# Performance work log

Measured on AMD Instinct MI355X. Metric: run time of the kernel, lower is better.

## Reference

```python
import jax, jax.numpy as jnp
import numpy as np

N, K, D = 131072, 1024, 128


def setup_inputs() -> dict:
    key = jax.random.key(0)
    k1, k2 = jax.random.split(key)
    latent = jax.random.normal(k1, (N, D), dtype=jnp.float32)
    coords = jax.random.uniform(k2, (K, D), dtype=jnp.float32)  # torch.rand init
    return {"latent": latent, "coords": coords}


def reference(latent, coords):
    # Euclidean cdist argmin: sqrt is monotone, so argmin of squared distances
    # matches torch.cdist(...).min(1)[1].
    x2 = jnp.sum(latent * latent, axis=1, keepdims=True)          # [N, 1]
    c2 = jnp.sum(coords * coords, axis=1)[None, :]                # [1, K]
    d2 = x2 + c2 - 2.0 * (latent @ coords.T)                      # [N, K]
    closest_centroid = jnp.argmin(d2, axis=1)                     # [N] int
    # original also computes cluster_distances but discards it; output is indices
    return closest_centroid
```

## Files before the change

### kernel.cpp

```cpp
#include <hip/hip_runtime.h>


constexpr int N = 131072;
constexpr int K = 1024;
constexpr int D = 128;
constexpr float EPS2 = 0.06f;

typedef __attribute__((ext_vector_type(8))) short short8;
typedef __attribute__((ext_vector_type(4))) float f32x4;

typedef const __attribute__((address_space(1))) uint* gas_uint;
typedef __attribute__((address_space(3))) uint* las_uint;

union U8 { uint4 u; short8 s; };
__device__ inline short8 as_s8(uint4 v) { U8 x; x.u = v; return x.s; }

__device__ inline uint bf16rne(float f) {
    uint u = __float_as_uint(f);
    return (u + 0x7fffu + ((u >> 16) & 1u)) >> 16;
}
__device__ inline void split2(float a, float b, uint& hi, uint& lo) {
    uint ha = bf16rne(a), hb = bf16rne(b);
    float la = a - __uint_as_float(ha << 16);
    float lb = b - __uint_as_float(hb << 16);
    hi = ha | (hb << 16);
    lo = bf16rne(la) | (bf16rne(lb) << 16);
}

__global__ __launch_bounds__(256) void prep_kernel(
    const float* __restrict__ coords, float* __restrict__ c2half,
    uint* __restrict__ chilo, int* __restrict__ counter) {
    if (blockIdx.x == 0 && threadIdx.x == 0) counter[0] = 0;
    const int k = blockIdx.x * 4 + (threadIdx.x >> 6);
    const int dw = threadIdx.x & 63;
    float a = coords[k * D + 2 * dw], b = coords[k * D + 2 * dw + 1];
    uint hi, lo;
    split2(a, b, hi, lo);
    const int g = dw >> 2, sub = dw & 3, kt = k >> 5, m = k & 31;
    char* base = (char*)chilo + (size_t)kt * 16384 + m * 256 +
                 ((g ^ (m & 15)) << 4) + sub * 4;
    *(uint*)base = hi;
    *(uint*)(base + 8192) = lo;
    float s = fmaf(a, a, b * b);
#pragma unroll
    for (int off = 1; off < 64; off <<= 1) s += __shfl_xor(s, off);
    if (dw == 0) c2half[k] = 0.5f * s;
}

__global__ __launch_bounds__(256) void transpose_kernel(
    const float* __restrict__ coords, float* __restrict__ coordsT) {
    __shared__ float tile[64][65];
    const int k0 = blockIdx.x * 64;
    const int d0 = blockIdx.y * 64;
    const int tx = threadIdx.x & 63, ty = threadIdx.x >> 6;
#pragma unroll
    for (int i = 0; i < 64; i += 4)
        tile[ty + i][tx] = coords[(size_t)(k0 + ty + i) * D + d0 + tx];
    __syncthreads();
#pragma unroll
    for (int i = 0; i < 64; i += 4)
        coordsT[(size_t)(d0 + ty + i) * K + k0 + tx] = tile[tx][ty + i];
}

__global__ __launch_bounds__(256, 3) void centroid_mfma_kernel(
    const float* __restrict__ latent, const uint* __restrict__ chilo,
    const float* __restrict__ c2, int* __restrict__ out,
    int* __restrict__ counter, int* __restrict__ list) {
    __shared__ __align__(16) char smem[36864];
    const int tid = threadIdx.x;
    const int l = tid & 63, w = tid >> 6;
    const int l15 = l & 15, l4 = l >> 4;
    const int rowbase = blockIdx.x * 128 + w * 32;

    uint4 bh[2][4], bl[2][4];
#pragma unroll
    for (int grp = 0; grp < 2; ++grp) {
        const float* rp =
            latent + (size_t)(rowbase + grp * 16 + l15) * D + l4 * 8;
#pragma unroll
        for (int s = 0; s < 4; ++s) {
            float4 u = *(const float4*)(rp + 32 * s);
            float4 v = *(const float4*)(rp + 32 * s + 4);
            uint h0, o0, h1, o1, h2, o2, h3, o3;
            split2(-u.x, -u.y, h0, o0);
            split2(-u.z, -u.w, h1, o1);
            split2(-v.x, -v.y, h2, o2);
            split2(-v.z, -v.w, h3, o3);
            bh[grp][s] = make_uint4(h0, h1, h2, h3);
            bl[grp][s] = make_uint4(o0, o1, o2, o3);
        }
    }
    *(float4*)(smem + 32768 + tid * 16) =
        *(const float4*)((const char*)c2 + tid * 16);

    const int w4096 = w << 12;
    const char* gsrc0 = (const char*)chilo + w4096 + ((tid & 63) << 4);
#pragma unroll
    for (int i = 0; i < 4; ++i)
        __builtin_amdgcn_global_load_lds((gas_uint)(gsrc0 + i * 1024),
                                         (las_uint)(smem + w4096 + i * 1024),
                                         16, 0, 0);
#pragma unroll
    for (int i = 0; i < 4; ++i)
        __builtin_amdgcn_global_load_lds((gas_uint)(gsrc0 + 16384 + i * 1024),
                                         (las_uint)(smem + 16384 + w4096 + i * 1024),
                                         16, 0, 0);
    __syncthreads();

    float m1[2] = {3.4e38f, 3.4e38f};
    float m2[2] = {3.4e38f, 3.4e38f};
    uint kpack[8];
#pragma unroll
    for (int ks = 0; ks < 2; ++ks)
#pragma unroll
        for (int r = 0; r < 4; ++r) kpack[ks * 4 + r] = ks * 16 + l4 * 4 + r;
    const float* c2l = (const float*)(smem + 32768);

#pragma unroll 1
    for (int t = 0; t < 32; ++t) {
        const int buf = t & 1;
        if (t < 31)
            asm volatile("s_waitcnt vmcnt(4)" ::: "memory");
        else
            asm volatile("s_waitcnt vmcnt(0)" ::: "memory");
        __builtin_amdgcn_s_barrier();
        __builtin_amdgcn_sched_barrier(0);

        const int k0 = t * 32;
        f32x4 acc[2][2];
#pragma unroll
        for (int ks = 0; ks < 2; ++ks) {
            float4 cq = *(const float4*)(c2l + k0 + ks * 16 + l4 * 4);
#pragma unroll
            for (int grp = 0; grp < 2; ++grp) {
                acc[ks][grp][0] = cq.x;
                acc[ks][grp][1] = cq.y;
                acc[ks][grp][2] = cq.z;
                acc[ks][grp][3] = cq.w;
            }
        }

        const char* lhs = smem + buf * 16384;
        __builtin_amdgcn_s_setprio(1);
#pragma unroll
        for (int s = 0; s < 4; ++s) {
            short8 ahi[2], alo[2];
#pragma unroll
            for (int ks = 0; ks < 2; ++ks) {
                const int m = ks * 16 + l15;
                const int g = l4 + 4 * s;
                const int sw = m * 256 + ((g ^ (m & 15)) << 4);
                ahi[ks] = *(const short8*)(lhs + sw);
                alo[ks] = *(const short8*)(lhs + 8192 + sw);
            }
#pragma unroll
            for (int ks = 0; ks < 2; ++ks) {
#pragma unroll
                for (int grp = 0; grp < 2; ++grp) {
                    acc[ks][grp] = __builtin_amdgcn_mfma_f32_16x16x32_bf16(
                        ahi[ks], as_s8(bh[grp][s]), acc[ks][grp], 0, 0, 0);
                    acc[ks][grp] = __builtin_amdgcn_mfma_f32_16x16x32_bf16(
                        ahi[ks], as_s8(bl[grp][s]), acc[ks][grp], 0, 0, 0);
                    acc[ks][grp] = __builtin_amdgcn_mfma_f32_16x16x32_bf16(
                        alo[ks], as_s8(bh[grp][s]), acc[ks][grp], 0, 0, 0);
                }
            }
        }
        __builtin_amdgcn_s_setprio(0);
        __builtin_amdgcn_sched_barrier(0);

#pragma unroll
        for (int ks = 0; ks < 2; ++ks) {
#pragma unroll
            for (int r = 0; r < 4; ++r) {
                const uint kk = kpack[ks * 4 + r];
#pragma unroll
                for (int grp = 0; grp < 2; ++grp) {
                    uint pb = (__float_as_uint(acc[ks][grp][r]) & 0xFFFFFC00u) | kk;
                    float vp = __uint_as_float(pb);
                    m2[grp] = __builtin_amdgcn_fmed3f(vp, m1[grp], m2[grp]);
                    m1[grp] = fminf(m1[grp], vp);
                }
            }
        }
#pragma unroll
        for (int i = 0; i < 8; ++i) kpack[i] += 32;

        __builtin_amdgcn_s_barrier();
        __builtin_amdgcn_sched_barrier(0);
        if (t < 30) {
            const char* gs = gsrc0 + (size_t)(t + 2) * 16384;
            char* ls = smem + buf * 16384 + w4096;
#pragma unroll
            for (int i = 0; i < 4; ++i)
                __builtin_amdgcn_global_load_lds((gas_uint)(gs + i * 1024),
                                                 (las_uint)(ls + i * 1024),
                                                 16, 0, 0);
        }
    }

#pragma unroll
    for (int off = 16; off <= 32; off <<= 1) {
#pragma unroll
        for (int grp = 0; grp < 2; ++grp) {
            float om = __shfl_xor(m1[grp], off);
            float o2 = __shfl_xor(m2[grp], off);
            m2[grp] = fminf(fminf(m2[grp], o2), fmaxf(m1[grp], om));
            m1[grp] = fminf(m1[grp], om);
        }
    }

    bool flg[2];
    unsigned long long bm[2];
    int total = 0;
#pragma unroll
    for (int grp = 0; grp < 2; ++grp) {
        flg[grp] = (l < 16) && ((m2[grp] - m1[grp]) <= EPS2);
        bm[grp] = __ballot(flg[grp]);
        total += __popcll(bm[grp]);
    }
    int pos = 0;
    if (l == 0 && total) pos = atomicAdd(counter, total);
    pos = __shfl(pos, 0);
    if (l < 16) {
        int run = pos;
#pragma unroll
        for (int grp = 0; grp < 2; ++grp) {
            out[rowbase + grp * 16 + l] = (int)(__float_as_uint(m1[grp]) & 1023u);
            if (flg[grp])
                list[run + __popcll(bm[grp] & ((1ull << l) - 1ull))] =
                    rowbase + grp * 16 + l;
            run += __popcll(bm[grp]);
        }
    }
}

__global__ __launch_bounds__(256) void centroid_exact_kernel(
    const float* __restrict__ latent, const float* __restrict__ coordsT,
    const float* __restrict__ c2, const int* __restrict__ cnt_list,
    int* __restrict__ out) {
    const int count = cnt_list[0];
    const int* list = cnt_list + 16;
    const int lane = threadIdx.x & 63;
    const int gw = (blockIdx.x * 256 + threadIdx.x) >> 6;
    const int nwaves = gridDim.x * 4;

    for (int task = gw; task * 4 < count; task += nwaves) {
        const int base = task * 4;
        const int nr = min(4, count - base);
        const float* xp[4];
        int rows[4];
#pragma unroll
        for (int j = 0; j < 4; ++j) {
            int idx = base + (j < nr ? j : nr - 1);
            rows[j] = __builtin_amdgcn_readfirstlane(list[idx]);
            xp[j] = latent + (size_t)rows[j] * D;
        }

        float acc[16][4];
#pragma unroll
        for (int c = 0; c < 16; ++c) {
            float cc = c2[c * 64 + lane];
#pragma unroll
            for (int j = 0; j < 4; ++j) acc[c][j] = cc;
        }

#pragma unroll 1
        for (int d4 = 0; d4 < D / 4; ++d4) {
            float4 xq[4];
#pragma unroll
            for (int j = 0; j < 4; ++j)
                xq[j] = *(const float4*)(xp[j] + 4 * d4);
            float ct[4][16];
#pragma unroll
            for (int dd = 0; dd < 4; ++dd)
#pragma unroll
                for (int c = 0; c < 16; ++c)
                    ct[dd][c] = coordsT[(size_t)(4 * d4 + dd) * K + c * 64 + lane];
#pragma unroll
            for (int dd = 0; dd < 4; ++dd) {
#pragma unroll
                for (int c = 0; c < 16; ++c) {
#pragma unroll
                    for (int j = 0; j < 4; ++j) {
                        float xv = (dd == 0) ? xq[j].x
                                 : (dd == 1) ? xq[j].y
                                 : (dd == 2) ? xq[j].z : xq[j].w;
                        acc[c][j] = fmaf(-xv, ct[dd][c], acc[c][j]);
                    }
                }
            }
        }

#pragma unroll
        for (int j = 0; j < 4; ++j) {
            float m1 = acc[0][j];
            int i1 = lane;
#pragma unroll
            for (int c = 1; c < 16; ++c) {
                const int kk = c * 64 + lane;
                if (acc[c][j] < m1) { m1 = acc[c][j]; i1 = kk; }
            }
#pragma unroll
            for (int off = 1; off < 64; off <<= 1) {
                float om = __shfl_xor(m1, off);
                int oi = __shfl_xor(i1, off);
                if (om < m1 || (om == m1 && oi < i1)) { m1 = om; i1 = oi; }
            }
            if (lane == 0 && j < nr) out[rows[j]] = i1;
        }
    }
}

extern "C" void kernel_launch(void* const* d_in, const int* in_sizes, int n_in,
                              void* d_out, int out_size, void* d_ws, size_t ws_size,
                              hipStream_t stream) {
    const float* latent = (const float*)d_in[0];
    const float* coords = (const float*)d_in[1];
    int* out = (int*)d_out;

    char* ws = (char*)d_ws;
    size_t off = 0;
    float* c2 = (float*)(ws + off); off += 4096;
    uint* chilo = (uint*)(ws + off); off += 524288;
    float* coordsT = (float*)(ws + off); off += 524288;
    int* cnt_list = (int*)(ws + off); off += 64 + 524288;
    int* counter = cnt_list;
    int* list = cnt_list + 16;

    prep_kernel<<<K / 4, 256, 0, stream>>>(coords, c2, chilo, counter);
    {
        dim3 g(K / 64, D / 64);
        transpose_kernel<<<g, 256, 0, stream>>>(coords, coordsT);
    }
    centroid_mfma_kernel<<<N / 128, 256, 0, stream>>>(latent, chilo, c2, out,
                                                      counter, list);
    centroid_exact_kernel<<<2048, 256, 0, stream>>>(latent, coordsT, c2,
                                                    cnt_list, out);
}
```

Baseline: 151.7 us.

## Switch distance MFMA to single fp16 pass with norm-scaled refine threshold

Replaces the three-pass bf16 hi/lo split GEMM with a single fp16 MFMA pass, which cuts the MFMA work to a third and halves the centroid tile traffic. Blocks become one wave owning 64 rows, so the per-tile workgroup barriers go away and each wave reuses each loaded centroid fragment across four row groups. The near-tie threshold for the exact fallback now scales with each row's norm to cover the larger fp16 error. The risks are more rows sent to the exact kernel and possible fp16 overflow or precision trouble on inputs with a different scale.

```diff
diff --git a/kernel.cpp b/kernel.cpp
--- a/kernel.cpp
+++ b/kernel.cpp
@@ -4,43 +4,35 @@
 constexpr int N = 131072;
 constexpr int K = 1024;
 constexpr int D = 128;
-constexpr float EPS2 = 0.06f;
-
-typedef __attribute__((ext_vector_type(8))) short short8;
+
+typedef __attribute__((ext_vector_type(8))) _Float16 half8;
 typedef __attribute__((ext_vector_type(4))) float f32x4;
 
 typedef const __attribute__((address_space(1))) uint* gas_uint;
 typedef __attribute__((address_space(3))) uint* las_uint;
 
-union U8 { uint4 u; short8 s; };
-__device__ inline short8 as_s8(uint4 v) { U8 x; x.u = v; return x.s; }
-
-__device__ inline uint bf16rne(float f) {
-    uint u = __float_as_uint(f);
-    return (u + 0x7fffu + ((u >> 16) & 1u)) >> 16;
-}
-__device__ inline void split2(float a, float b, uint& hi, uint& lo) {
-    uint ha = bf16rne(a), hb = bf16rne(b);
-    float la = a - __uint_as_float(ha << 16);
-    float lb = b - __uint_as_float(hb << 16);
-    hi = ha | (hb << 16);
-    lo = bf16rne(la) | (bf16rne(lb) << 16);
+union UH { uint4 u; half8 h; };
+__device__ inline half8 as_h8(uint4 v) { UH x; x.u = v; return x.h; }
+
+union H2U { _Float16 h[2]; uint u; };
+__device__ inline uint fp16pk(float a, float b) {
+    H2U x;
+    x.h[0] = (_Float16)a;
+    x.h[1] = (_Float16)b;
+    return x.u;
 }
 
 __global__ __launch_bounds__(256) void prep_kernel(
     const float* __restrict__ coords, float* __restrict__ c2half,
-    uint* __restrict__ chilo, int* __restrict__ counter) {
+    uint* __restrict__ chi, int* __restrict__ counter) {
     if (blockIdx.x == 0 && threadIdx.x == 0) counter[0] = 0;
     const int k = blockIdx.x * 4 + (threadIdx.x >> 6);
     const int dw = threadIdx.x & 63;
     float a = coords[k * D + 2 * dw], b = coords[k * D + 2 * dw + 1];
-    uint hi, lo;
-    split2(a, b, hi, lo);
     const int g = dw >> 2, sub = dw & 3, kt = k >> 5, m = k & 31;
-    char* base = (char*)chilo + (size_t)kt * 16384 + m * 256 +
+    char* base = (char*)chi + (size_t)kt * 8192 + m * 256 +
                  ((g ^ (m & 15)) << 4) + sub * 4;
-    *(uint*)base = hi;
-    *(uint*)(base + 8192) = lo;
+    *(uint*)base = fp16pk(a, b);
     float s = fmaf(a, a, b * b);
 #pragma unroll
     for (int off = 1; off < 64; off <<= 1) s += __shfl_xor(s, off);
@@ -62,77 +54,82 @@
         coordsT[(size_t)(d0 + ty + i) * K + k0 + tx] = tile[tx][ty + i];
 }
 
-__global__ __launch_bounds__(256, 3) void centroid_mfma_kernel(
-    const float* __restrict__ latent, const uint* __restrict__ chilo,
+__global__ __launch_bounds__(64, 2) void centroid_mfma_kernel(
+    const float* __restrict__ latent, const uint* __restrict__ chi,
     const float* __restrict__ c2, int* __restrict__ out,
     int* __restrict__ counter, int* __restrict__ list) {
-    __shared__ __align__(16) char smem[36864];
-    const int tid = threadIdx.x;
-    const int l = tid & 63, w = tid >> 6;
+    __shared__ __align__(16) char smem[20480];
+    const int l = threadIdx.x;
     const int l15 = l & 15, l4 = l >> 4;
-    const int rowbase = blockIdx.x * 128 + w * 32;
-
-    uint4 bh[2][4], bl[2][4];
-#pragma unroll
-    for (int grp = 0; grp < 2; ++grp) {
+    const int rowbase = blockIdx.x * 64;
+
+    uint4 bh[4][4];
+    float n2[4];
+#pragma unroll
+    for (int grp = 0; grp < 4; ++grp) {
         const float* rp =
             latent + (size_t)(rowbase + grp * 16 + l15) * D + l4 * 8;
+        float s2 = 0.f;
 #pragma unroll
         for (int s = 0; s < 4; ++s) {
             float4 u = *(const float4*)(rp + 32 * s);
             float4 v = *(const float4*)(rp + 32 * s + 4);
-            uint h0, o0, h1, o1, h2, o2, h3, o3;
-            split2(-u.x, -u.y, h0, o0);
-            split2(-u.z, -u.w, h1, o1);
-            split2(-v.x, -v.y, h2, o2);
-            split2(-v.z, -v.w, h3, o3);
-            bh[grp][s] = make_uint4(h0, h1, h2, h3);
-            bl[grp][s] = make_uint4(o0, o1, o2, o3);
-        }
-    }
-    *(float4*)(smem + 32768 + tid * 16) =
-        *(const float4*)((const char*)c2 + tid * 16);
-
-    const int w4096 = w << 12;
-    const char* gsrc0 = (const char*)chilo + w4096 + ((tid & 63) << 4);
-#pragma unroll
-    for (int i = 0; i < 4; ++i)
+            s2 += u.x * u.x + u.y * u.y + u.z * u.z + u.w * u.w +
+                  v.x * v.x + v.y * v.y + v.z * v.z + v.w * v.w;
+            bh[grp][s] = make_uint4(fp16pk(-u.x, -u.y), fp16pk(-u.z, -u.w),
+                                    fp16pk(-v.x, -v.y), fp16pk(-v.z, -v.w));
+        }
+        n2[grp] = s2;
+    }
+#pragma unroll
+    for (int grp = 0; grp < 4; ++grp) {
+        n2[grp] += __shfl_xor(n2[grp], 16);
+        n2[grp] += __shfl_xor(n2[grp], 32);
+    }
+
+    {
+        float4* dst = (float4*)(smem + 16384);
+        const float4* src = (const float4*)c2;
+#pragma unroll
+        for (int i = 0; i < 4; ++i) dst[i * 64 + l] = src[i * 64 + l];
+    }
+
+    const char* gsrc0 = (const char*)chi + (l << 4);
+#pragma unroll
+    for (int i = 0; i < 8; ++i)
         __builtin_amdgcn_global_load_lds((gas_uint)(gsrc0 + i * 1024),
-                                         (las_uint)(smem + w4096 + i * 1024),
+                                         (las_uint)(smem + i * 1024), 16, 0, 0);
+#pragma unroll
+    for (int i = 0; i < 8; ++i)
+        __builtin_amdgcn_global_load_lds((gas_uint)(gsrc0 + 8192 + i * 1024),
+                                         (las_uint)(smem + 8192 + i * 1024),
                                          16, 0, 0);
-#pragma unroll
-    for (int i = 0; i < 4; ++i)
-        __builtin_amdgcn_global_load_lds((gas_uint)(gsrc0 + 16384 + i * 1024),
-                                         (las_uint)(smem + 16384 + w4096 + i * 1024),
-                                         16, 0, 0);
-    __syncthreads();
-
-    float m1[2] = {3.4e38f, 3.4e38f};
-    float m2[2] = {3.4e38f, 3.4e38f};
+
+    float m1[4] = {3.4e38f, 3.4e38f, 3.4e38f, 3.4e38f};
+    float m2[4] = {3.4e38f, 3.4e38f, 3.4e38f, 3.4e38f};
     uint kpack[8];
 #pragma unroll
     for (int ks = 0; ks < 2; ++ks)
 #pragma unroll
         for (int r = 0; r < 4; ++r) kpack[ks * 4 + r] = ks * 16 + l4 * 4 + r;
-    const float* c2l = (const float*)(smem + 32768);
+    const float* c2l = (const float*)(smem + 16384);
 
 #pragma unroll 1
     for (int t = 0; t < 32; ++t) {
         const int buf = t & 1;
         if (t < 31)
-            asm volatile("s_waitcnt vmcnt(4)" ::: "memory");
+            asm volatile("s_waitcnt vmcnt(8)" ::: "memory");
         else
             asm volatile("s_waitcnt vmcnt(0)" ::: "memory");
-        __builtin_amdgcn_s_barrier();
         __builtin_amdgcn_sched_barrier(0);
 
         const int k0 = t * 32;
-        f32x4 acc[2][2];
+        f32x4 acc[2][4];
 #pragma unroll
         for (int ks = 0; ks < 2; ++ks) {
             float4 cq = *(const float4*)(c2l + k0 + ks * 16 + l4 * 4);
 #pragma unroll
-            for (int grp = 0; grp < 2; ++grp) {
+            for (int grp = 0; grp < 4; ++grp) {
                 acc[ks][grp][0] = cq.x;
                 acc[ks][grp][1] = cq.y;
                 acc[ks][grp][2] = cq.z;
@@ -140,31 +137,23 @@
             }
         }
 
-        const char* lhs = smem + buf * 16384;
+        const char* lhs = smem + buf * 8192;
         __builtin_amdgcn_s_setprio(1);
 #pragma unroll
         for (int s = 0; s < 4; ++s) {
-            short8 ahi[2], alo[2];
+            half8 a[2];
 #pragma unroll
             for (int ks = 0; ks < 2; ++ks) {
                 const int m = ks * 16 + l15;
                 const int g = l4 + 4 * s;
-                const int sw = m * 256 + ((g ^ (m & 15)) << 4);
-                ahi[ks] = *(const short8*)(lhs + sw);
-                alo[ks] = *(const short8*)(lhs + 8192 + sw);
-            }
-#pragma unroll
-            for (int ks = 0; ks < 2; ++ks) {
-#pragma unroll
-                for (int grp = 0; grp < 2; ++grp) {
-                    acc[ks][grp] = __builtin_amdgcn_mfma_f32_16x16x32_bf16(
-                        ahi[ks], as_s8(bh[grp][s]), acc[ks][grp], 0, 0, 0);
-                    acc[ks][grp] = __builtin_amdgcn_mfma_f32_16x16x32_bf16(
-                        ahi[ks], as_s8(bl[grp][s]), acc[ks][grp], 0, 0, 0);
-                    acc[ks][grp] = __builtin_amdgcn_mfma_f32_16x16x32_bf16(
-                        alo[ks], as_s8(bh[grp][s]), acc[ks][grp], 0, 0, 0);
-                }
-            }
+                a[ks] = *(const half8*)(lhs + m * 256 + ((g ^ (m & 15)) << 4));
+            }
+#pragma unroll
+            for (int ks = 0; ks < 2; ++ks)
+#pragma unroll
+                for (int grp = 0; grp < 4; ++grp)
+                    acc[ks][grp] = __builtin_amdgcn_mfma_f32_16x16x32_f16(
+                        a[ks], as_h8(bh[grp][s]), acc[ks][grp], 0, 0, 0);
         }
         __builtin_amdgcn_s_setprio(0);
         __builtin_amdgcn_sched_barrier(0);
@@ -175,7 +164,7 @@
             for (int r = 0; r < 4; ++r) {
                 const uint kk = kpack[ks * 4 + r];
 #pragma unroll
-                for (int grp = 0; grp < 2; ++grp) {
+                for (int grp = 0; grp < 4; ++grp) {
                     uint pb = (__float_as_uint(acc[ks][grp][r]) & 0xFFFFFC00u) | kk;
                     float vp = __uint_as_float(pb);
                     m2[grp] = __builtin_amdgcn_fmed3f(vp, m1[grp], m2[grp]);
@@ -186,13 +175,13 @@
 #pragma unroll
         for (int i = 0; i < 8; ++i) kpack[i] += 32;
 
-        __builtin_amdgcn_s_barrier();
+        asm volatile("s_waitcnt lgkmcnt(0)" ::: "memory");
         __builtin_amdgcn_sched_barrier(0);
         if (t < 30) {
-            const char* gs = gsrc0 + (size_t)(t + 2) * 16384;
-            char* ls = smem + buf * 16384 + w4096;
-#pragma unroll
-            for (int i = 0; i < 4; ++i)
+            const char* gs = gsrc0 + (size_t)(t + 2) * 8192;
+            char* ls = smem + buf * 8192;
+#pragma unroll
+            for (int i = 0; i < 8; ++i)
                 __builtin_amdgcn_global_load_lds((gas_uint)(gs + i * 1024),
                                                  (las_uint)(ls + i * 1024),
                                                  16, 0, 0);
@@ -202,7 +191,7 @@
 #pragma unroll
     for (int off = 16; off <= 32; off <<= 1) {
 #pragma unroll
-        for (int grp = 0; grp < 2; ++grp) {
+        for (int grp = 0; grp < 4; ++grp) {
             float om = __shfl_xor(m1[grp], off);
             float o2 = __shfl_xor(m2[grp], off);
             m2[grp] = fminf(fminf(m2[grp], o2), fmaxf(m1[grp], om));
@@ -210,12 +199,13 @@
         }
     }
 
-    bool flg[2];
-    unsigned long long bm[2];
+    bool flg[4];
+    unsigned long long bm[4];
     int total = 0;
 #pragma unroll
-    for (int grp = 0; grp < 2; ++grp) {
-        flg[grp] = (l < 16) && ((m2[grp] - m1[grp]) <= EPS2);
+    for (int grp = 0; grp < 4; ++grp) {
+        float eps = 0.0276f * sqrtf(n2[grp]) + 0.042f;
+        flg[grp] = (l < 16) && ((m2[grp] - m1[grp]) <= eps);
         bm[grp] = __ballot(flg[grp]);
         total += __popcll(bm[grp]);
     }
@@ -225,7 +215,7 @@
     if (l < 16) {
         int run = pos;
 #pragma unroll
-        for (int grp = 0; grp < 2; ++grp) {
+        for (int grp = 0; grp < 4; ++grp) {
             out[rowbase + grp * 16 + l] = (int)(__float_as_uint(m1[grp]) & 1023u);
             if (flg[grp])
                 list[run + __popcll(bm[grp] & ((1ull << l) - 1ull))] =
@@ -322,19 +312,19 @@
     char* ws = (char*)d_ws;
     size_t off = 0;
     float* c2 = (float*)(ws + off); off += 4096;
-    uint* chilo = (uint*)(ws + off); off += 524288;
+    uint* chi = (uint*)(ws + off); off += 262144;
     float* coordsT = (float*)(ws + off); off += 524288;
     int* cnt_list = (int*)(ws + off); off += 64 + 524288;
     int* counter = cnt_list;
     int* list = cnt_list + 16;
 
-    prep_kernel<<<K / 4, 256, 0, stream>>>(coords, c2, chilo, counter);
+    prep_kernel<<<K / 4, 256, 0, stream>>>(coords, c2, chi, counter);
     {
         dim3 g(K / 64, D / 64);
         transpose_kernel<<<g, 256, 0, stream>>>(coords, coordsT);
     }
-    centroid_mfma_kernel<<<N / 128, 256, 0, stream>>>(latent, chilo, c2, out,
-                                                      counter, list);
+    centroid_mfma_kernel<<<N / 64, 64, 0, stream>>>(latent, chi, c2, out,
+                                                    counter, list);
     centroid_exact_kernel<<<2048, 256, 0, stream>>>(latent, coordsT, c2,
                                                     cnt_list, out);
 }
```

Measured after the change: 245.6 us. 1.62x slower.
